# Kernel optimization log

Measured on AMD Instinct MI355X. Metric: run time of the kernel, lower is better.

The kernel has to match this reference:

```python
import jax, jax.numpy as jnp
import numpy as np

B, S, D, N, L, V = 2, 512, 1024, 4096, 4, 32000
EPS = 1e-5

def ternarize(w):
    # BitNet b1.58-style: scale = mean |w|, quantize to {-1,0,1}, rescale.
    s = jnp.mean(jnp.abs(w)) + 1e-8
    return s * jnp.round(jnp.clip(w / s, -1.0, 1.0))

def tern_ste(w):
    # straight-through estimator (faithful to ternary training)
    return w + jax.lax.stop_gradient(ternarize(w) - w)

def layer_norm(x, g, b):
    mu = jnp.mean(x, axis=-1, keepdims=True)
    var = jnp.var(x, axis=-1, keepdims=True)
    return (x - mu) * jax.lax.rsqrt(var + EPS) * g + b

def setup_inputs() -> dict:
    key = jax.random.key(0)
    ks = jax.random.split(key, 20)
    sc = lambda d: 1.0 / np.sqrt(d)
    inp = {
        'input_ids': jax.random.randint(ks[0], (B, S), 0, V, dtype=jnp.int32),
        'emb':       jax.random.normal(ks[1], (V, D), jnp.float32) * 0.02,
        'pos_emb':   jax.random.normal(ks[2], (S, D), jnp.float32) * 0.02,
        'gru_wih':   jax.random.normal(ks[3], (3 * D, D), jnp.float32) * sc(D),
        'gru_whh':   jax.random.normal(ks[4], (3 * D, D), jnp.float32) * sc(D),
        'gru_bih':   jnp.zeros((3 * D,), jnp.float32),
        'gru_bhh':   jnp.zeros((3 * D,), jnp.float32),
        'syn_w':     jax.random.normal(ks[5], (L, N, D), jnp.float32) * sc(D),
        'syn_b':     jnp.zeros((L, N), jnp.float32),
        'out_w':     jax.random.normal(ks[6], (L, D, N), jnp.float32) * sc(N),
        'out_b':     jnp.zeros((L, D), jnp.float32),
        'ln_g':      jnp.ones((L, D), jnp.float32),
        'ln_b':      jnp.zeros((L, D), jnp.float32),
        'on_g':      jnp.ones((D,), jnp.float32),
        'on_b':      jnp.zeros((D,), jnp.float32),
        'head_w':    jax.random.normal(ks[7], (V, D), jnp.float32) * sc(D),
        'head_b':    jnp.zeros((V,), jnp.float32),
    }
    return inp

def gru(x, wih, whh, bih, bhh):
    # x: [B,S,D] -> [B,S,D], torch nn.GRU semantics, h0 = 0
    # Precompute input projections for all timesteps: [B,S,3D]
    gi_all = jnp.einsum('bsd,ed->bse', x, wih) + bih
    def step(h, gi):
        gh = h @ whh.T + bhh
        ir, iz, inn = jnp.split(gi, 3, axis=-1)
        hr, hz, hn = jnp.split(gh, 3, axis=-1)
        r = jax.nn.sigmoid(ir + hr)
        z = jax.nn.sigmoid(iz + hz)
        n = jnp.tanh(inn + r * hn)
        h_new = (1.0 - z) * n + z * h
        return h_new, h_new
    h0 = jnp.zeros((x.shape[0], whh.shape[1]), x.dtype)
    _, hs = jax.lax.scan(step, h0, jnp.swapaxes(gi_all, 0, 1))
    return jnp.swapaxes(hs, 0, 1)

def reference(input_ids, emb, pos_emb, gru_wih, gru_whh, gru_bih, gru_bhh,
              syn_w, syn_b, out_w, out_b, ln_g, ln_b, on_g, on_b,
              head_w, head_b):
    # Ternary embedding lookup
    x = tern_ste(emb)[input_ids]                       # [B,S,D]
    x = x + pos_emb[None, :x.shape[1], :]
    x = gru(x, gru_wih, gru_whh, gru_bih, gru_bhh)
    for l in range(L):
        residual = x
        hidden = jax.nn.relu(jnp.einsum('bsd,nd->bsn', x, tern_ste(syn_w[l])) + syn_b[l])
        out = jnp.einsum('bsn,dn->bsd', hidden, tern_ste(out_w[l])) + out_b[l]
        x = layer_norm(residual + out, ln_g[l], ln_b[l])
    x = layer_norm(x, on_g, on_b)
    logits = jnp.einsum('bsd,vd->bsv', x, tern_ste(head_w)) + head_b  # [B,S,V]
    return logits
```

## Files before the change

### kernel.cpp

```cpp
#include <hip/hip_runtime.h>
#include <hip/hip_bf16.h>
#include <cstdint>
#include <cstddef>

#define Dm 1024
#define Sm 512
#define Bm 2
#define Nm 4096
#define Lm 4
#define Vm 32000

typedef __attribute__((ext_vector_type(8))) short short8;
typedef __attribute__((ext_vector_type(4))) float floatx4;

__device__ __forceinline__ unsigned short f2b(float f){
  union { float f; unsigned u; } v; v.f = f;
  unsigned r = (v.u + 0x7fffu + ((v.u >> 16) & 1u)) >> 16;
  return (unsigned short)r;
}
__device__ __forceinline__ float b2f(unsigned short h){
  union { unsigned u; float f; } v; v.u = ((unsigned)h) << 16;
  return v.f;
}

__global__ __launch_bounds__(256) void absum_all_kernel(
    const float* __restrict__ emb, const float* __restrict__ syn_w,
    const float* __restrict__ out_w, const float* __restrict__ head_w,
    double* __restrict__ partial)
{
  int wid = blockIdx.x >> 7;
  int blk = blockIdx.x & 127;
  const float* base; long n4;
  if (wid == 0){ base = emb; n4 = (long)Vm * Dm / 4; }
  else if (wid <= 4){ base = syn_w + (size_t)(wid - 1) * Nm * Dm; n4 = (long)Nm * Dm / 4; }
  else if (wid <= 8){ base = out_w + (size_t)(wid - 5) * Dm * Nm; n4 = (long)Nm * Dm / 4; }
  else { base = head_w; n4 = (long)Vm * Dm / 4; }

  long i = (long)blk * 256 + threadIdx.x;
  const long stride = 128L * 256;
  double s = 0.0;
  for (; i < n4; i += stride){
    float4 v = ((const float4*)base)[i];
    s += (double)fabsf(v.x) + (double)fabsf(v.y) + (double)fabsf(v.z) + (double)fabsf(v.w);
  }
  #pragma unroll
  for (int off = 32; off; off >>= 1) s += __shfl_down(s, off, 64);
  __shared__ double wsum[4];
  int lane = threadIdx.x & 63, wv = threadIdx.x >> 6;
  if (lane == 0) wsum[wv] = s;
  __syncthreads();
  if (threadIdx.x == 0) partial[wid * 128 + blk] = wsum[0] + wsum[1] + wsum[2] + wsum[3];
}

__global__ __launch_bounds__(128) void scale_kernel(const double* __restrict__ partials,
                                                    float* __restrict__ scales){
  int b = blockIdx.x;
  int tid = threadIdx.x;
  __shared__ double red[128];
  red[tid] = partials[b * 128 + tid];
  __syncthreads();
  for (int off = 64; off; off >>= 1){
    if (tid < off) red[tid] += red[tid + off];
    __syncthreads();
  }
  if (tid == 0){
    double cnt = (b == 0 || b == 9) ? (double)Vm * (double)Dm : (double)Nm * (double)Dm;
    scales[b] = (float)(red[0] / cnt);
  }
}

__global__ __launch_bounds__(256) void tern_kernel(const float* __restrict__ w,
                                                   const float* __restrict__ smean,
                                                   unsigned short* __restrict__ out, long n4){
  float s = smean[0] + 1e-8f;
  long i = (long)blockIdx.x * blockDim.x + threadIdx.x;
  long stride = (long)gridDim.x * blockDim.x;
  for (; i < n4; i += stride){
    float4 v = ((const float4*)w)[i];
    ushort4 o;
    o.x = f2b(rintf(fminf(fmaxf(v.x / s, -1.f), 1.f)));
    o.y = f2b(rintf(fminf(fmaxf(v.y / s, -1.f), 1.f)));
    o.z = f2b(rintf(fminf(fmaxf(v.z / s, -1.f), 1.f)));
    o.w = f2b(rintf(fminf(fmaxf(v.w / s, -1.f), 1.f)));
    ((ushort4*)out)[i] = o;
  }
}

__global__ __launch_bounds__(256) void split_kernel(const float* __restrict__ w,
                                                    unsigned short* __restrict__ hi,
                                                    unsigned short* __restrict__ lo, long n4){
  long i = (long)blockIdx.x * blockDim.x + threadIdx.x;
  long stride = (long)gridDim.x * blockDim.x;
  for (; i < n4; i += stride){
    float4 v = ((const float4*)w)[i];
    float f[4] = {v.x, v.y, v.z, v.w};
    ushort4 h4, l4;
    unsigned short* hp = (unsigned short*)&h4;
    unsigned short* lp = (unsigned short*)&l4;
    #pragma unroll
    for (int e = 0; e < 4; e++){
      unsigned short h = f2b(f[e]);
      hp[e] = h;
      lp[e] = f2b(f[e] - b2f(h));
    }
    ((ushort4*)hi)[i] = h4;
    ((ushort4*)lo)[i] = l4;
  }
}

__global__ __launch_bounds__(256) void embed_kernel(
    const int* __restrict__ ids, const float* __restrict__ emb,
    const float* __restrict__ pos, const float* __restrict__ smean,
    unsigned short* __restrict__ xhi, unsigned short* __restrict__ xlo)
{
  int row = blockIdx.x;
  int sp  = row & (Sm - 1);
  int id  = ids[row];
  float s = smean[0] + 1e-8f;
  int d = threadIdx.x * 4;
  float4 wv = *(const float4*)(emb + (size_t)id * Dm + d);
  float4 pv = *(const float4*)(pos + (size_t)sp * Dm + d);
  float y[4];
  y[0] = s * rintf(fminf(fmaxf(wv.x / s, -1.f), 1.f)) + pv.x;
  y[1] = s * rintf(fminf(fmaxf(wv.y / s, -1.f), 1.f)) + pv.y;
  y[2] = s * rintf(fminf(fmaxf(wv.z / s, -1.f), 1.f)) + pv.z;
  y[3] = s * rintf(fminf(fmaxf(wv.w / s, -1.f), 1.f)) + pv.w;
  ushort4 h4, l4;
  unsigned short* hp = (unsigned short*)&h4;
  unsigned short* lp = (unsigned short*)&l4;
  #pragma unroll
  for (int e = 0; e < 4; e++){
    unsigned short h = f2b(y[e]);
    hp[e] = h;
    lp[e] = f2b(y[e] - b2f(h));
  }
  size_t base = (size_t)row * Dm + d;
  *(ushort4*)(xhi + base) = h4;
  *(ushort4*)(xlo + base) = l4;
}

template<bool WSPLIT, bool WF32, int BT>
__global__ __launch_bounds__(256) void gemm_kernel(
    const unsigned short* __restrict__ Ahi, const unsigned short* __restrict__ Alo,
    const void* __restrict__ Wsrc, const unsigned short* __restrict__ Wlo,
    const float* __restrict__ bias, const float* __restrict__ smean,
    int relu, float* __restrict__ outf,
    unsigned short* __restrict__ outhi, unsigned short* __restrict__ outlo,
    int M, int N, int K)
{
  constexpr int WT = BT / 2;
  constexpr int FT = WT / 16;
  constexpr int RPT = 256 / BT;
  constexpr int CPT = 32 / RPT;
  constexpr int NU  = CPT / 8;

  __shared__ unsigned short As[2][BT][40];
  __shared__ unsigned short Bs[WSPLIT ? 2 : 1][BT][40];
  int tid = threadIdx.x;
  int wave = tid >> 6, lane = tid & 63;
  int wm = wave >> 1, wn = wave & 1;
  int bm = blockIdx.y, bn = blockIdx.x;

  bool tern = (smean != nullptr);
  float s = 1.f;
  if (tern) s = smean[0] + 1e-8f;

  int arow = tid / RPT, sub = tid % RPT;
  int col0 = sub * CPT;
  const unsigned short* Agh = Ahi + (size_t)(bm * BT + arow) * K + col0;
  const unsigned short* Agl = Alo + (size_t)(bm * BT + arow) * K + col0;
  const float* Wgf = nullptr;
  const unsigned short* Wgh = nullptr;
  const unsigned short* Wgl = nullptr;
  if (WF32) Wgf = (const float*)Wsrc + (size_t)(bn * BT + arow) * K + col0;
  else {
    Wgh = (const unsigned short*)Wsrc + (size_t)(bn * BT + arow) * K + col0;
    if (WSPLIT) Wgl = Wlo + (size_t)(bn * BT + arow) * K + col0;
  }

  floatx4 acc[FT][FT];
  #pragma unroll
  for (int i = 0; i < FT; i++)
    #pragma unroll
    for (int j = 0; j < FT; j++)
      acc[i][j] = (floatx4){0.f, 0.f, 0.f, 0.f};

  int kpb = K / (int)gridDim.z;
  int k_beg = blockIdx.z * kpb;

  for (int k0 = k_beg; k0 < k_beg + kpb; k0 += 32){
    __syncthreads();
    #pragma unroll
    for (int u = 0; u < NU; u++){
      *(uint4*)&As[0][arow][col0 + u * 8] = *(const uint4*)(Agh + k0 + u * 8);
      *(uint4*)&As[1][arow][col0 + u * 8] = *(const uint4*)(Agl + k0 + u * 8);
    }
    if (WF32){
      unsigned short tmp[CPT];
      #pragma unroll
      for (int q = 0; q < CPT / 4; q++){
        float4 wv = *(const float4*)(Wgf + k0 + q * 4);
        float f[4] = {wv.x, wv.y, wv.z, wv.w};
        #pragma unroll
        for (int e = 0; e < 4; e++){
          float w = f[e];
          if (tern) w = rintf(fminf(fmaxf(w / s, -1.f), 1.f));
          tmp[q * 4 + e] = f2b(w);
        }
      }
      #pragma unroll
      for (int u = 0; u < NU; u++)
        *(uint4*)&Bs[0][arow][col0 + u * 8] = *(uint4*)&tmp[u * 8];
    } else {
      #pragma unroll
      for (int u = 0; u < NU; u++){
        *(uint4*)&Bs[0][arow][col0 + u * 8] = *(const uint4*)(Wgh + k0 + u * 8);
        if (WSPLIT)
          *(uint4*)&Bs[1][arow][col0 + u * 8] = *(const uint4*)(Wgl + k0 + u * 8);
      }
    }
    __syncthreads();

    int kq = lane >> 4, mr = lane & 15;
    short8 afh[FT], afl[FT], bfh[FT];
    #pragma unroll
    for (int i = 0; i < FT; i++){
      afh[i] = *(const short8*)&As[0][wm*WT + i*16 + mr][kq*8];
      afl[i] = *(const short8*)&As[1][wm*WT + i*16 + mr][kq*8];
    }
    #pragma unroll
    for (int j = 0; j < FT; j++) bfh[j] = *(const short8*)&Bs[0][wn*WT + j*16 + mr][kq*8];
    #pragma unroll
    for (int i = 0; i < FT; i++)
      #pragma unroll
      for (int j = 0; j < FT; j++){
        acc[i][j] = __builtin_amdgcn_mfma_f32_16x16x32_bf16(afh[i], bfh[j], acc[i][j], 0, 0, 0);
        acc[i][j] = __builtin_amdgcn_mfma_f32_16x16x32_bf16(afl[i], bfh[j], acc[i][j], 0, 0, 0);
      }
    if (WSPLIT){
      short8 bfl[FT];
      #pragma unroll
      for (int j = 0; j < FT; j++) bfl[j] = *(const short8*)&Bs[1][wn*WT + j*16 + mr][kq*8];
      #pragma unroll
      for (int i = 0; i < FT; i++)
        #pragma unroll
        for (int j = 0; j < FT; j++)
          acc[i][j] = __builtin_amdgcn_mfma_f32_16x16x32_bf16(afh[i], bfl[j], acc[i][j], 0, 0, 0);
    }
  }

  bool split = (gridDim.z > 1);
  bool addb = (blockIdx.z == 0);
  int cr = lane >> 4, cc = lane & 15;
  #pragma unroll
  for (int j = 0; j < FT; j++){
    int col = bn * BT + wn * WT + j * 16 + cc;
    float bv = (bias && addb) ? bias[col] : 0.f;
    #pragma unroll
    for (int i = 0; i < FT; i++){
      #pragma unroll
      for (int r = 0; r < 4; r++){
        int row = bm * BT + wm * WT + i * 16 + cr * 4 + r;
        float v = acc[i][j][r] * s + bv;
        if (relu) v = fmaxf(v, 0.f);
        size_t idx = (size_t)row * N + col;
        if (outf){
          if (split) atomicAdd(outf + idx, v);
          else outf[idx] = v;
        }
        if (outhi){
          unsigned short h = f2b(v);
          outhi[idx] = h;
          outlo[idx] = f2b(v - b2f(h));
        }
      }
    }
  }
}

__global__ __launch_bounds__(1024) void gru_kernel(
    const float* __restrict__ gi, const float* __restrict__ whh, const float* __restrict__ bhh,
    unsigned long long* __restrict__ hbuf, float* __restrict__ hs,
    unsigned short* __restrict__ xhi, unsigned short* __restrict__ xlo)
{
  __shared__ float lds_h[2 * 1088];
  __shared__ float lds_gh[96];
  int w = blockIdx.x, tid = threadIdx.x;
  int d0 = w * 16;
  int o = tid >> 4, c = tid & 15;
  bool active = (o < 48);
  int g = o >> 4, dl = o & 15;
  int wrow = g * Dm + d0 + dl;
  float wreg[64];
  if (active){
    const float* src = whh + (size_t)wrow * Dm + c * 64;
    #pragma unroll
    for (int i = 0; i < 64; i++) wreg[i] = src[i];
  }
  float bhval = active ? bhh[wrow] : 0.f;

  int bb = tid >> 4, dd = tid & 15;
  float hprev = 0.f;

  for (int t = 0; t < Sm; t++){
    float ir = 0.f, iz = 0.f, inn = 0.f;
    if (tid < 32){
      const float* girow = gi + ((size_t)bb * Sm + t) * (3 * Dm);
      int d = d0 + dd;
      ir  = girow[d];
      iz  = girow[Dm + d];
      inn = girow[2 * Dm + d];
    }
    {
      const unsigned long long* src = hbuf + (size_t)(t & 1) * 2048 + tid * 2;
      unsigned got = 0;
      int spins = 0;
      while (got != 3u){
        #pragma unroll
        for (int q = 0; q < 2; q++){
          if (!(got & (1u << q))){
            unsigned long long wd = __hip_atomic_load(src + q, __ATOMIC_RELAXED,
                                                      __HIP_MEMORY_SCOPE_AGENT);
            if ((unsigned)(wd >> 32) == (unsigned)t){
              union { unsigned u; float f; } cv; cv.u = (unsigned)wd;
              int wi = tid * 2 + q;
              int b = wi >> 10, d = wi & 1023;
              lds_h[b * 1088 + (d >> 6) * 68 + (d & 63)] = cv.f;
              got |= 1u << q;
            }
          }
        }
        if (got != 3u){
          if (++spins > (1 << 20)) break;
          __builtin_amdgcn_s_sleep(1);
        }
      }
    }
    __syncthreads();
    if (active){
      const float* hp = lds_h + c * 68;
      float a0 = 0.f, a1 = 0.f;
      #pragma unroll
      for (int i = 0; i < 64; i++){
        float wv = wreg[i];
        a0 += wv * hp[i];
        a1 += wv * hp[1088 + i];
      }
      #pragma unroll
      for (int off = 8; off; off >>= 1){
        a0 += __shfl_xor(a0, off, 16);
        a1 += __shfl_xor(a1, off, 16);
      }
      if (c == 0){
        lds_gh[o]      = a0 + bhval;
        lds_gh[48 + o] = a1 + bhval;
      }
    }
    __syncthreads();
    if (tid < 32){
      float gr = lds_gh[bb * 48 + dd];
      float gz = lds_gh[bb * 48 + 16 + dd];
      float gn = lds_gh[bb * 48 + 32 + dd];
      float rr = 1.f / (1.f + expf(-(ir + gr)));
      float zz = 1.f / (1.f + expf(-(iz + gz)));
      float nn = tanhf(inn + rr * gn);
      float hnew = (1.f - zz) * nn + zz * hprev;
      hprev = hnew;
      int d = d0 + dd;
      union { float f; unsigned u; } cv; cv.f = hnew;
      unsigned long long wd = ((unsigned long long)(unsigned)(t + 1) << 32) | (unsigned long long)cv.u;
      __hip_atomic_store(hbuf + (size_t)((t + 1) & 1) * 2048 + bb * Dm + d, wd,
                         __ATOMIC_RELAXED, __HIP_MEMORY_SCOPE_AGENT);
      size_t oi = ((size_t)bb * Sm + t) * Dm + d;
      hs[oi] = hnew;
      unsigned short h = f2b(hnew);
      xhi[oi] = h;
      xlo[oi] = f2b(hnew - b2f(h));
    }
  }
}

__global__ __launch_bounds__(256) void ln_kernel(
    const float* __restrict__ resid, const float* __restrict__ addv,
    const float* __restrict__ g, const float* __restrict__ b,
    float* __restrict__ outf, unsigned short* __restrict__ outhi,
    unsigned short* __restrict__ outlo)
{
  int row = blockIdx.x;
  int d = threadIdx.x * 4;
  size_t base = (size_t)row * Dm + d;
  float4 v = *(const float4*)(resid + base);
  if (addv){
    float4 a = *(const float4*)(addv + base);
    v.x += a.x; v.y += a.y; v.z += a.z; v.w += a.w;
  }
  float sum = v.x + v.y + v.z + v.w;
  float sq  = v.x*v.x + v.y*v.y + v.z*v.z + v.w*v.w;
  #pragma unroll
  for (int off = 32; off; off >>= 1){
    sum += __shfl_down(sum, off, 64);
    sq  += __shfl_down(sq,  off, 64);
  }
  __shared__ float red[4][2];
  __shared__ float bc[2];
  int lane = threadIdx.x & 63, wv = threadIdx.x >> 6;
  if (lane == 0){ red[wv][0] = sum; red[wv][1] = sq; }
  __syncthreads();
  if (threadIdx.x == 0){
    float st = red[0][0] + red[1][0] + red[2][0] + red[3][0];
    float qt = red[0][1] + red[1][1] + red[2][1] + red[3][1];
    float mu = st * (1.f / Dm);
    float var = qt * (1.f / Dm) - mu * mu;
    bc[0] = mu; bc[1] = rsqrtf(var + 1e-5f);
  }
  __syncthreads();
  float mu = bc[0], rs = bc[1];
  float4 gv = *(const float4*)(g + d);
  float4 bv = *(const float4*)(b + d);
  float y[4];
  y[0] = (v.x - mu) * rs * gv.x + bv.x;
  y[1] = (v.y - mu) * rs * gv.y + bv.y;
  y[2] = (v.z - mu) * rs * gv.z + bv.z;
  y[3] = (v.w - mu) * rs * gv.w + bv.w;
  if (outf) *(float4*)(outf + base) = *(float4*)y;
  if (outhi){
    ushort4 h4, l4;
    unsigned short* hp = (unsigned short*)&h4;
    unsigned short* lp = (unsigned short*)&l4;
    #pragma unroll
    for (int e = 0; e < 4; e++){
      unsigned short h = f2b(y[e]);
      hp[e] = h;
      lp[e] = f2b(y[e] - b2f(h));
    }
    *(ushort4*)(outhi + base) = h4;
    *(ushort4*)(outlo + base) = l4;
  }
}

extern "C" void kernel_launch(void* const* d_in, const int* in_sizes, int n_in,
                              void* d_out, int out_size, void* d_ws, size_t ws_size,
                              hipStream_t stream)
{
  const int*   ids    = (const int*)  d_in[0];
  const float* emb    = (const float*)d_in[1];
  const float* pos    = (const float*)d_in[2];
  const float* wih    = (const float*)d_in[3];
  const float* whh    = (const float*)d_in[4];
  const float* bih    = (const float*)d_in[5];
  const float* bhh    = (const float*)d_in[6];
  const float* syn_w  = (const float*)d_in[7];
  const float* syn_b  = (const float*)d_in[8];
  const float* out_w  = (const float*)d_in[9];
  const float* out_b  = (const float*)d_in[10];
  const float* ln_g   = (const float*)d_in[11];
  const float* ln_b   = (const float*)d_in[12];
  const float* on_g   = (const float*)d_in[13];
  const float* on_b   = (const float*)d_in[14];
  const float* head_w = (const float*)d_in[15];
  const float* head_b = (const float*)d_in[16];
  float* logits = (float*)d_out;

  const size_t MB = (size_t)1 << 20;
  char* ws = (char*)d_ws;
  float*  scales   = (float*) ws;
  double* partials = (double*)(ws + 32768);
  unsigned long long* hbuf = (unsigned long long*)(ws + 131072);
  float*          hs     = (float*)         (ws + 1  * MB);
  unsigned short* xhi    = (unsigned short*)(ws + 5  * MB);
  unsigned short* xlo    = (unsigned short*)(ws + 7  * MB);
  float*          outbuf = (float*)         (ws + 9  * MB);
  float*          gi     = (float*)         (ws + 13 * MB);
  unsigned short* wih_hi = (unsigned short*)(ws + 25 * MB);
  unsigned short* wih_lo = (unsigned short*)(ws + 31 * MB);
  unsigned short* hhi    = (unsigned short*)(ws + 37 * MB);
  unsigned short* hlo    = (unsigned short*)(ws + 45 * MB);
  unsigned short* wbuf   = (unsigned short*)(ws + 53 * MB);

  bool pre_layer = ws_size >= 62  * MB;
  bool pre_head  = ws_size >= 120 * MB;

  hipMemsetAsync(d_ws, 0, 163840, stream);

  absum_all_kernel<<<1280, 256, 0, stream>>>(emb, syn_w, out_w, head_w, partials);
  scale_kernel<<<10, 128, 0, stream>>>(partials, scales);

  embed_kernel<<<1024, 256, 0, stream>>>(ids, emb, pos, scales, xhi, xlo);

  split_kernel<<<2048, 256, 0, stream>>>(wih, wih_hi, wih_lo, (long)(3 * Dm) * Dm / 4);
  gemm_kernel<true, false, 64><<<dim3(3072/64, 1024/64, 1), 256, 0, stream>>>(
      xhi, xlo, wih_hi, wih_lo, bih, nullptr, 0, gi, nullptr, nullptr, 1024, 3072, 1024);

  gru_kernel<<<64, 1024, 0, stream>>>(gi, whh, bhh, hbuf, hs, xhi, xlo);

  for (int l = 0; l < Lm; l++){
    if (pre_layer){
      tern_kernel<<<2048, 256, 0, stream>>>(syn_w + (size_t)l * Nm * Dm, scales + 1 + l,
                                            wbuf, (long)Nm * Dm / 4);
      gemm_kernel<false, false, 64><<<dim3(4096/64, 1024/64, 1), 256, 0, stream>>>(
          xhi, xlo, wbuf, nullptr, syn_b + (size_t)l * Nm, scales + 1 + l,
          1, nullptr, hhi, hlo, 1024, 4096, 1024);
    } else {
      gemm_kernel<false, true, 64><<<dim3(4096/64, 1024/64, 1), 256, 0, stream>>>(
          xhi, xlo, syn_w + (size_t)l * Nm * Dm, nullptr, syn_b + (size_t)l * Nm, scales + 1 + l,
          1, nullptr, hhi, hlo, 1024, 4096, 1024);
    }
    hipMemsetAsync(outbuf, 0, (size_t)1024 * 1024 * 4, stream);
    if (pre_layer){
      tern_kernel<<<2048, 256, 0, stream>>>(out_w + (size_t)l * Dm * Nm, scales + 5 + l,
                                            wbuf, (long)Dm * Nm / 4);
      gemm_kernel<false, false, 64><<<dim3(1024/64, 1024/64, 2), 256, 0, stream>>>(
          hhi, hlo, wbuf, nullptr, out_b + (size_t)l * Dm, scales + 5 + l,
          0, outbuf, nullptr, nullptr, 1024, 1024, 4096);
    } else {
      gemm_kernel<false, true, 64><<<dim3(1024/64, 1024/64, 2), 256, 0, stream>>>(
          hhi, hlo, out_w + (size_t)l * Dm * Nm, nullptr, out_b + (size_t)l * Dm, scales + 5 + l,
          0, outbuf, nullptr, nullptr, 1024, 1024, 4096);
    }
    ln_kernel<<<1024, 256, 0, stream>>>(hs, outbuf, ln_g + (size_t)l * Dm, ln_b + (size_t)l * Dm,
                                        hs, xhi, xlo);
  }
  ln_kernel<<<1024, 256, 0, stream>>>(hs, nullptr, on_g, on_b, nullptr, xhi, xlo);

  if (pre_head){
    tern_kernel<<<2048, 256, 0, stream>>>(head_w, scales + 9, wbuf, (long)Vm * Dm / 4);
    gemm_kernel<false, false, 128><<<dim3(32000/128, 1024/128, 1), 256, 0, stream>>>(
        xhi, xlo, wbuf, nullptr, head_b, scales + 9, 0, logits, nullptr, nullptr, 1024, 32000, 1024);
  } else {
    gemm_kernel<false, true, 128><<<dim3(32000/128, 1024/128, 1), 256, 0, stream>>>(
        xhi, xlo, head_w, nullptr, head_b, scales + 9, 0, logits, nullptr, nullptr, 1024, 32000, 1024);
  }
}
```

Measured before the change: 2.224 ms.

## Add direct global-to-LDS GEMM with swizzled layout and 128 tiles

Adds a new GEMM kernel that loads A and W tiles straight from global memory into LDS using global_load_lds. It uses an XOR-swizzled layout to avoid bank conflicts and larger 128x128 tiles for the pre-ternarized bf16 paths (GRU input projection, layer GEMMs, head). The aim is to cut register staging and VGPR traffic on tile loads and to get more reuse per block. The fp32-weight fallback keeps the old kernel. It risks fewer blocks in flight for the 1024x1024 GEMMs and stays single-buffered, so the loads are not overlapped with compute.

Result: slower. 2.331 ms (+4.8%).

```diff
diff --git a/kernel.cpp b/kernel.cpp
--- a/kernel.cpp
+++ b/kernel.cpp
@@ -21,6 +21,12 @@
 __device__ __forceinline__ float b2f(unsigned short h){
   union { unsigned u; float f; } v; v.u = ((unsigned)h) << 16;
   return v.f;
+}
+
+__device__ __forceinline__ void gload16(const unsigned short* g, unsigned short* l){
+  __builtin_amdgcn_global_load_lds(
+      (const __attribute__((address_space(1))) void*)g,
+      (__attribute__((address_space(3))) void*)l, 16, 0, 0);
 }
 
 __global__ __launch_bounds__(256) void absum_all_kernel(
@@ -139,10 +145,138 @@
   *(ushort4*)(xlo + base) = l4;
 }
 
-template<bool WSPLIT, bool WF32, int BT>
+template<bool WSPLIT>
+__global__ __launch_bounds__(256) void gemm_lds_kernel(
+    const unsigned short* __restrict__ Ahi, const unsigned short* __restrict__ Alo,
+    const unsigned short* __restrict__ Whi, const unsigned short* __restrict__ Wlo,
+    const float* __restrict__ bias, const float* __restrict__ smean,
+    int relu, float* __restrict__ outf,
+    unsigned short* __restrict__ outhi, unsigned short* __restrict__ outlo,
+    int M, int N, int K)
+{
+  constexpr int NP = WSPLIT ? 4 : 3;
+  __shared__ __align__(16) unsigned short lds[NP * 4096];
+  int tid = threadIdx.x;
+  int wave = tid >> 6, lane = tid & 63;
+  int wm = wave >> 1, wn = wave & 1;
+  int bm = blockIdx.y, bn = blockIdx.x;
+
+  float s = 1.f;
+  if (smean) s = smean[0] + 1e-8f;
+
+  int r0 = wave * 32 + (lane >> 2);
+  int r1 = r0 + 16;
+  int s0 = (lane & 3) ^ ((r0 >> 1) & 3);
+  int s1 = (lane & 3) ^ ((r1 >> 1) & 3);
+  const unsigned short* ga0 = Ahi + (size_t)(bm * 128 + r0) * K + s0 * 8;
+  const unsigned short* ga1 = Ahi + (size_t)(bm * 128 + r1) * K + s1 * 8;
+  const unsigned short* gl0 = Alo + (size_t)(bm * 128 + r0) * K + s0 * 8;
+  const unsigned short* gl1 = Alo + (size_t)(bm * 128 + r1) * K + s1 * 8;
+  const unsigned short* gw0 = Whi + (size_t)(bn * 128 + r0) * K + s0 * 8;
+  const unsigned short* gw1 = Whi + (size_t)(bn * 128 + r1) * K + s1 * 8;
+  const unsigned short* gv0 = nullptr;
+  const unsigned short* gv1 = nullptr;
+  if (WSPLIT){
+    gv0 = Wlo + (size_t)(bn * 128 + r0) * K + s0 * 8;
+    gv1 = Wlo + (size_t)(bn * 128 + r1) * K + s1 * 8;
+  }
+  unsigned short* la = &lds[wave * 1024];
+
+  floatx4 acc[4][4];
+  #pragma unroll
+  for (int i = 0; i < 4; i++)
+    #pragma unroll
+    for (int j = 0; j < 4; j++)
+      acc[i][j] = (floatx4){0.f, 0.f, 0.f, 0.f};
+
+  int kpb = K / (int)gridDim.z;
+  int k_beg = (int)blockIdx.z * kpb;
+
+  for (int k0 = k_beg; k0 < k_beg + kpb; k0 += 32){
+    __syncthreads();
+    gload16(ga0 + k0, la);
+    gload16(ga1 + k0, la + 512);
+    gload16(gl0 + k0, la + 4096);
+    gload16(gl1 + k0, la + 4096 + 512);
+    gload16(gw0 + k0, la + 8192);
+    gload16(gw1 + k0, la + 8192 + 512);
+    if (WSPLIT){
+      gload16(gv0 + k0, la + 12288);
+      gload16(gv1 + k0, la + 12288 + 512);
+    }
+    __syncthreads();
+
+    int kq = lane >> 4, mr = lane & 15;
+    short8 afh[4], afl[4], bfh[4];
+    #pragma unroll
+    for (int i = 0; i < 4; i++){
+      int r = wm * 64 + i * 16 + mr;
+      int off = r * 32 + ((kq ^ ((r >> 1) & 3)) << 3);
+      afh[i] = *(const short8*)&lds[off];
+      afl[i] = *(const short8*)&lds[4096 + off];
+    }
+    #pragma unroll
+    for (int j = 0; j < 4; j++){
+      int r = wn * 64 + j * 16 + mr;
+      int off = r * 32 + ((kq ^ ((r >> 1) & 3)) << 3);
+      bfh[j] = *(const short8*)&lds[8192 + off];
+    }
+    #pragma unroll
+    for (int i = 0; i < 4; i++)
+      #pragma unroll
+      for (int j = 0; j < 4; j++){
+        acc[i][j] = __builtin_amdgcn_mfma_f32_16x16x32_bf16(afh[i], bfh[j], acc[i][j], 0, 0, 0);
+        acc[i][j] = __builtin_amdgcn_mfma_f32_16x16x32_bf16(afl[i], bfh[j], acc[i][j], 0, 0, 0);
+      }
+    if (WSPLIT){
+      short8 bfl[4];
+      #pragma unroll
+      for (int j = 0; j < 4; j++){
+        int r = wn * 64 + j * 16 + mr;
+        int off = r * 32 + ((kq ^ ((r >> 1) & 3)) << 3);
+        bfl[j] = *(const short8*)&lds[12288 + off];
+      }
+      #pragma unroll
+      for (int i = 0; i < 4; i++)
+        #pragma unroll
+        for (int j = 0; j < 4; j++)
+          acc[i][j] = __builtin_amdgcn_mfma_f32_16x16x32_bf16(afh[i], bfl[j], acc[i][j], 0, 0, 0);
+    }
+  }
+
+  bool split = (gridDim.z > 1);
+  bool addb = (blockIdx.z == 0);
+  int cr = lane >> 4, cc = lane & 15;
+  #pragma unroll
+  for (int j = 0; j < 4; j++){
+    int col = bn * 128 + wn * 64 + j * 16 + cc;
+    float bv = (bias && addb) ? bias[col] : 0.f;
+    #pragma unroll
+    for (int i = 0; i < 4; i++){
+      #pragma unroll
+      for (int r = 0; r < 4; r++){
+        int row = bm * 128 + wm * 64 + i * 16 + cr * 4 + r;
+        float v = acc[i][j][r] * s + bv;
+        if (relu) v = fmaxf(v, 0.f);
+        size_t idx = (size_t)row * N + col;
+        if (outf){
+          if (split) atomicAdd(outf + idx, v);
+          else outf[idx] = v;
+        }
+        if (outhi){
+          unsigned short h = f2b(v);
+          outhi[idx] = h;
+          outlo[idx] = f2b(v - b2f(h));
+        }
+      }
+    }
+  }
+}
+
+template<int BT>
 __global__ __launch_bounds__(256) void gemm_kernel(
     const unsigned short* __restrict__ Ahi, const unsigned short* __restrict__ Alo,
-    const void* __restrict__ Wsrc, const unsigned short* __restrict__ Wlo,
+    const float* __restrict__ Wsrc,
     const float* __restrict__ bias, const float* __restrict__ smean,
     int relu, float* __restrict__ outf,
     unsigned short* __restrict__ outhi, unsigned short* __restrict__ outlo,
@@ -155,7 +289,7 @@
   constexpr int NU  = CPT / 8;
 
   __shared__ unsigned short As[2][BT][40];
-  __shared__ unsigned short Bs[WSPLIT ? 2 : 1][BT][40];
+  __shared__ unsigned short Bs[BT][40];
   int tid = threadIdx.x;
   int wave = tid >> 6, lane = tid & 63;
   int wm = wave >> 1, wn = wave & 1;
@@ -169,14 +303,7 @@
   int col0 = sub * CPT;
   const unsigned short* Agh = Ahi + (size_t)(bm * BT + arow) * K + col0;
   const unsigned short* Agl = Alo + (size_t)(bm * BT + arow) * K + col0;
-  const float* Wgf = nullptr;
-  const unsigned short* Wgh = nullptr;
-  const unsigned short* Wgl = nullptr;
-  if (WF32) Wgf = (const float*)Wsrc + (size_t)(bn * BT + arow) * K + col0;
-  else {
-    Wgh = (const unsigned short*)Wsrc + (size_t)(bn * BT + arow) * K + col0;
-    if (WSPLIT) Wgl = Wlo + (size_t)(bn * BT + arow) * K + col0;
-  }
+  const float* Wgf = Wsrc + (size_t)(bn * BT + arow) * K + col0;
 
   floatx4 acc[FT][FT];
   #pragma unroll
@@ -195,7 +322,7 @@
       *(uint4*)&As[0][arow][col0 + u * 8] = *(const uint4*)(Agh + k0 + u * 8);
       *(uint4*)&As[1][arow][col0 + u * 8] = *(const uint4*)(Agl + k0 + u * 8);
     }
-    if (WF32){
+    {
       unsigned short tmp[CPT];
       #pragma unroll
       for (int q = 0; q < CPT / 4; q++){
@@ -210,14 +337,7 @@
       }
       #pragma unroll
       for (int u = 0; u < NU; u++)
-        *(uint4*)&Bs[0][arow][col0 + u * 8] = *(uint4*)&tmp[u * 8];
-    } else {
-      #pragma unroll
-      for (int u = 0; u < NU; u++){
-        *(uint4*)&Bs[0][arow][col0 + u * 8] = *(const uint4*)(Wgh + k0 + u * 8);
-        if (WSPLIT)
-          *(uint4*)&Bs[1][arow][col0 + u * 8] = *(const uint4*)(Wgl + k0 + u * 8);
-      }
+        *(uint4*)&Bs[arow][col0 + u * 8] = *(uint4*)&tmp[u * 8];
     }
     __syncthreads();
 
@@ -229,7 +349,7 @@
       afl[i] = *(const short8*)&As[1][wm*WT + i*16 + mr][kq*8];
     }
     #pragma unroll
-    for (int j = 0; j < FT; j++) bfh[j] = *(const short8*)&Bs[0][wn*WT + j*16 + mr][kq*8];
+    for (int j = 0; j < FT; j++) bfh[j] = *(const short8*)&Bs[wn*WT + j*16 + mr][kq*8];
     #pragma unroll
     for (int i = 0; i < FT; i++)
       #pragma unroll
@@ -237,16 +357,6 @@
         acc[i][j] = __builtin_amdgcn_mfma_f32_16x16x32_bf16(afh[i], bfh[j], acc[i][j], 0, 0, 0);
         acc[i][j] = __builtin_amdgcn_mfma_f32_16x16x32_bf16(afl[i], bfh[j], acc[i][j], 0, 0, 0);
       }
-    if (WSPLIT){
-      short8 bfl[FT];
-      #pragma unroll
-      for (int j = 0; j < FT; j++) bfl[j] = *(const short8*)&Bs[1][wn*WT + j*16 + mr][kq*8];
-      #pragma unroll
-      for (int i = 0; i < FT; i++)
-        #pragma unroll
-        for (int j = 0; j < FT; j++)
-          acc[i][j] = __builtin_amdgcn_mfma_f32_16x16x32_bf16(afh[i], bfl[j], acc[i][j], 0, 0, 0);
-    }
   }
 
   bool split = (gridDim.z > 1);
@@ -488,7 +598,7 @@
   embed_kernel<<<1024, 256, 0, stream>>>(ids, emb, pos, scales, xhi, xlo);
 
   split_kernel<<<2048, 256, 0, stream>>>(wih, wih_hi, wih_lo, (long)(3 * Dm) * Dm / 4);
-  gemm_kernel<true, false, 64><<<dim3(3072/64, 1024/64, 1), 256, 0, stream>>>(
+  gemm_lds_kernel<true><<<dim3(3072/128, 1024/128, 1), 256, 0, stream>>>(
       xhi, xlo, wih_hi, wih_lo, bih, nullptr, 0, gi, nullptr, nullptr, 1024, 3072, 1024);
 
   gru_kernel<<<64, 1024, 0, stream>>>(gi, whh, bhh, hbuf, hs, xhi, xlo);
@@ -497,24 +607,24 @@
     if (pre_layer){
       tern_kernel<<<2048, 256, 0, stream>>>(syn_w + (size_t)l * Nm * Dm, scales + 1 + l,
                                             wbuf, (long)Nm * Dm / 4);
-      gemm_kernel<false, false, 64><<<dim3(4096/64, 1024/64, 1), 256, 0, stream>>>(
+      gemm_lds_kernel<false><<<dim3(4096/128, 1024/128, 1), 256, 0, stream>>>(
           xhi, xlo, wbuf, nullptr, syn_b + (size_t)l * Nm, scales + 1 + l,
           1, nullptr, hhi, hlo, 1024, 4096, 1024);
     } else {
-      gemm_kernel<false, true, 64><<<dim3(4096/64, 1024/64, 1), 256, 0, stream>>>(
-          xhi, xlo, syn_w + (size_t)l * Nm * Dm, nullptr, syn_b + (size_t)l * Nm, scales + 1 + l,
+      gemm_kernel<64><<<dim3(4096/64, 1024/64, 1), 256, 0, stream>>>(
+          xhi, xlo, syn_w + (size_t)l * Nm * Dm, syn_b + (size_t)l * Nm, scales + 1 + l,
           1, nullptr, hhi, hlo, 1024, 4096, 1024);
     }
     hipMemsetAsync(outbuf, 0, (size_t)1024 * 1024 * 4, stream);
     if (pre_layer){
       tern_kernel<<<2048, 256, 0, stream>>>(out_w + (size_t)l * Dm * Nm, scales + 5 + l,
                                             wbuf, (long)Dm * Nm / 4);
-      gemm_kernel<false, false, 64><<<dim3(1024/64, 1024/64, 2), 256, 0, stream>>>(
+      gemm_lds_kernel<false><<<dim3(1024/128, 1024/128, 2), 256, 0, stream>>>(
           hhi, hlo, wbuf, nullptr, out_b + (size_t)l * Dm, scales + 5 + l,
           0, outbuf, nullptr, nullptr, 1024, 1024, 4096);
     } else {
-      gemm_kernel<false, true, 64><<<dim3(1024/64, 1024/64, 2), 256, 0, stream>>>(
-          hhi, hlo, out_w + (size_t)l * Dm * Nm, nullptr, out_b + (size_t)l * Dm, scales + 5 + l,
+      gemm_kernel<64><<<dim3(1024/64, 1024/64, 2), 256, 0, stream>>>(
+          hhi, hlo, out_w + (size_t)l * Dm * Nm, out_b + (size_t)l * Dm, scales + 5 + l,
           0, outbuf, nullptr, nullptr, 1024, 1024, 4096);
     }
     ln_kernel<<<1024, 256, 0, stream>>>(hs, outbuf, ln_g + (size_t)l * Dm, ln_b + (size_t)l * Dm,
@@ -524,10 +634,10 @@
 
   if (pre_head){
     tern_kernel<<<2048, 256, 0, stream>>>(head_w, scales + 9, wbuf, (long)Vm * Dm / 4);
-    gemm_kernel<false, false, 128><<<dim3(32000/128, 1024/128, 1), 256, 0, stream>>>(
+    gemm_lds_kernel<false><<<dim3(32000/128, 1024/128, 1), 256, 0, stream>>>(
         xhi, xlo, wbuf, nullptr, head_b, scales + 9, 0, logits, nullptr, nullptr, 1024, 32000, 1024);
   } else {
-    gemm_kernel<false, true, 128><<<dim3(32000/128, 1024/128, 1), 256, 0, stream>>>(
-        xhi, xlo, head_w, nullptr, head_b, scales + 9, 0, logits, nullptr, nullptr, 1024, 32000, 1024);
-  }
-}
+    gemm_kernel<128><<<dim3(32000/128, 1024/128, 1), 256, 0, stream>>>(
+        xhi, xlo, head_w, head_b, scales + 9, 0, logits, nullptr, nullptr, 1024, 32000, 1024);
+  }
+}
```

## Add LDS-staged head GEMM using direct global-to-LDS loads with swizzle

Applied to the files above, without the earlier changes.

Adds a new GEMM kernel for the vocabulary head that stages A-hi, A-lo and ternarized weight tiles into shared memory with global_load_lds 16-byte transfers. It uses an XOR swizzle to avoid bank conflicts and runs bf16 MFMA 16x16x32 on the tiles. The aim is to cut global memory traffic and register-path loads in the largest GEMM through tile reuse across waves. It is single-buffered with two barriers per K step, so load latency may not be hidden, and it only runs when the pre_head path is taken.

After: 2.170 ms. -2.4%, faster.

```diff
diff --git a/kernel.cpp b/kernel.cpp
--- a/kernel.cpp
+++ b/kernel.cpp
@@ -21,6 +21,12 @@
 __device__ __forceinline__ float b2f(unsigned short h){
   union { unsigned u; float f; } v; v.u = ((unsigned)h) << 16;
   return v.f;
+}
+
+__device__ __forceinline__ void gload16(const unsigned short* g, unsigned short* l){
+  __builtin_amdgcn_global_load_lds(
+      (const __attribute__((address_space(1))) void*)g,
+      (__attribute__((address_space(3))) void*)l, 16, 0, 0);
 }
 
 __global__ __launch_bounds__(256) void absum_all_kernel(
@@ -278,6 +284,92 @@
   }
 }
 
+__global__ __launch_bounds__(256) void gemm_lds_kernel(
+    const unsigned short* __restrict__ Ahi, const unsigned short* __restrict__ Alo,
+    const unsigned short* __restrict__ Whi,
+    const float* __restrict__ bias, const float* __restrict__ smean,
+    int relu, float* __restrict__ outf, int M, int N, int K)
+{
+  __shared__ __align__(16) unsigned short lds[3 * 4096];
+  int tid = threadIdx.x;
+  int wave = tid >> 6, lane = tid & 63;
+  int wm = wave >> 1, wn = wave & 1;
+  int bm = blockIdx.y, bn = blockIdx.x;
+
+  float s = 1.f;
+  if (smean) s = smean[0] + 1e-8f;
+
+  int r0 = wave * 32 + (lane >> 2);
+  int r1 = r0 + 16;
+  int s0 = (lane & 3) ^ ((r0 >> 1) & 3);
+  int s1 = (lane & 3) ^ ((r1 >> 1) & 3);
+  const unsigned short* ga0 = Ahi + (size_t)(bm * 128 + r0) * K + s0 * 8;
+  const unsigned short* ga1 = Ahi + (size_t)(bm * 128 + r1) * K + s1 * 8;
+  const unsigned short* gl0 = Alo + (size_t)(bm * 128 + r0) * K + s0 * 8;
+  const unsigned short* gl1 = Alo + (size_t)(bm * 128 + r1) * K + s1 * 8;
+  const unsigned short* gw0 = Whi + (size_t)(bn * 128 + r0) * K + s0 * 8;
+  const unsigned short* gw1 = Whi + (size_t)(bn * 128 + r1) * K + s1 * 8;
+  unsigned short* la = &lds[wave * 1024];
+
+  floatx4 acc[4][4];
+  #pragma unroll
+  for (int i = 0; i < 4; i++)
+    #pragma unroll
+    for (int j = 0; j < 4; j++)
+      acc[i][j] = (floatx4){0.f, 0.f, 0.f, 0.f};
+
+  for (int k0 = 0; k0 < K; k0 += 32){
+    __syncthreads();
+    gload16(ga0 + k0, la);
+    gload16(ga1 + k0, la + 512);
+    gload16(gl0 + k0, la + 4096);
+    gload16(gl1 + k0, la + 4096 + 512);
+    gload16(gw0 + k0, la + 8192);
+    gload16(gw1 + k0, la + 8192 + 512);
+    __syncthreads();
+
+    int kq = lane >> 4, mr = lane & 15;
+    short8 afh[4], afl[4], bfh[4];
+    #pragma unroll
+    for (int i = 0; i < 4; i++){
+      int r = wm * 64 + i * 16 + mr;
+      int off = r * 32 + ((kq ^ ((r >> 1) & 3)) << 3);
+      afh[i] = *(const short8*)&lds[off];
+      afl[i] = *(const short8*)&lds[4096 + off];
+    }
+    #pragma unroll
+    for (int j = 0; j < 4; j++){
+      int r = wn * 64 + j * 16 + mr;
+      int off = r * 32 + ((kq ^ ((r >> 1) & 3)) << 3);
+      bfh[j] = *(const short8*)&lds[8192 + off];
+    }
+    #pragma unroll
+    for (int i = 0; i < 4; i++)
+      #pragma unroll
+      for (int j = 0; j < 4; j++){
+        acc[i][j] = __builtin_amdgcn_mfma_f32_16x16x32_bf16(afh[i], bfh[j], acc[i][j], 0, 0, 0);
+        acc[i][j] = __builtin_amdgcn_mfma_f32_16x16x32_bf16(afl[i], bfh[j], acc[i][j], 0, 0, 0);
+      }
+  }
+
+  int cr = lane >> 4, cc = lane & 15;
+  #pragma unroll
+  for (int j = 0; j < 4; j++){
+    int col = bn * 128 + wn * 64 + j * 16 + cc;
+    float bv = bias ? bias[col] : 0.f;
+    #pragma unroll
+    for (int i = 0; i < 4; i++){
+      #pragma unroll
+      for (int r = 0; r < 4; r++){
+        int row = bm * 128 + wm * 64 + i * 16 + cr * 4 + r;
+        float v = acc[i][j][r] * s + bv;
+        if (relu) v = fmaxf(v, 0.f);
+        outf[(size_t)row * N + col] = v;
+      }
+    }
+  }
+}
+
 __global__ __launch_bounds__(1024) void gru_kernel(
     const float* __restrict__ gi, const float* __restrict__ whh, const float* __restrict__ bhh,
     unsigned long long* __restrict__ hbuf, float* __restrict__ hs,
@@ -524,8 +616,8 @@
 
   if (pre_head){
     tern_kernel<<<2048, 256, 0, stream>>>(head_w, scales + 9, wbuf, (long)Vm * Dm / 4);
-    gemm_kernel<false, false, 128><<<dim3(32000/128, 1024/128, 1), 256, 0, stream>>>(
-        xhi, xlo, wbuf, nullptr, head_b, scales + 9, 0, logits, nullptr, nullptr, 1024, 32000, 1024);
+    gemm_lds_kernel<<<dim3(32000/128, 1024/128, 1), 256, 0, stream>>>(
+        xhi, xlo, wbuf, head_b, scales + 9, 0, logits, 1024, 32000, 1024);
   } else {
     gemm_kernel<false, true, 128><<<dim3(32000/128, 1024/128, 1), 256, 0, stream>>>(
         xhi, xlo, head_w, nullptr, head_b, scales + 9, 0, logits, nullptr, nullptr, 1024, 32000, 1024);
```
